# Kernel optimization log

Hardware: AMD Instinct MI355X
Metric: run time of the kernel (lower is better)

The kernel has to match this reference:

```python
import jax, jax.numpy as jnp
import numpy as np

INF = 1.0e9
# 8-connected neighborhood (Warcraft shortest-path convention)
DIRS = [(-1, -1), (-1, 0), (-1, 1), (0, -1), (0, 1), (1, -1), (1, 0), (1, 1)]


def _shifted(d_KGG, di, dj):
    # shifted[i, j] = d[i + di, j + dj], INF out of bounds (di, dj static ints)
    K, G, _ = d_KGG.shape
    p = jnp.pad(d_KGG, ((0, 0), (1, 1), (1, 1)), constant_values=INF)
    return p[:, 1 + di:1 + di + G, 1 + dj:1 + dj + G]


def compute_shortest_path(cost_KGG):
    """Vertex-cost shortest path from (0,0) to (G-1,G-1) on an 8-connected grid.
    Returns a 0/1 mask of cells on the optimal path. Bellman-Ford style DP:
    G*G relaxation sweeps guarantee convergence for positive costs."""
    K, G, _ = cost_KGG.shape
    dist0 = jnp.full((K, G, G), INF, dtype=cost_KGG.dtype).at[:, 0, 0].set(cost_KGG[:, 0, 0])

    def relax(_, dist):
        nbr = dist  # placeholder; fold min over 8 shifted copies
        nbr = _shifted(dist, *DIRS[0])
        for d in DIRS[1:]:
            nbr = jnp.minimum(nbr, _shifted(dist, *d))
        return jnp.minimum(dist, cost_KGG + nbr)

    dist = jax.lax.fori_loop(0, G * G, relax, dist0)

    # Backtrack from (G-1, G-1): predecessor = argmin dist over 8 neighbors.
    di = jnp.array([d[0] for d in DIRS])
    dj = jnp.array([d[1] for d in DIRS])
    ks = jnp.arange(K)

    def step(carry, _):
        mask, pi, pj = carry
        ci = pi[:, None] + di[None, :]   # [K, 8]
        cj = pj[:, None] + dj[None, :]
        valid = (ci >= 0) & (ci < G) & (cj >= 0) & (cj < G)
        cic = jnp.clip(ci, 0, G - 1)
        cjc = jnp.clip(cj, 0, G - 1)
        nd = jnp.where(valid, dist[ks[:, None], cic, cjc], INF)
        best = jnp.argmin(nd, axis=-1)  # [K]
        npi = jnp.take_along_axis(cic, best[:, None], 1)[:, 0]
        npj = jnp.take_along_axis(cjc, best[:, None], 1)[:, 0]
        done = (pi == 0) & (pj == 0)
        pi2 = jnp.where(done, pi, npi)
        pj2 = jnp.where(done, pj, npj)
        mask2 = mask.at[ks, pi2, pj2].set(1.0)
        return (mask2, pi2, pj2), None

    mask0 = jnp.zeros((K, G, G), jnp.float32).at[:, G - 1, G - 1].set(1.0)
    p0 = jnp.full((K,), G - 1, dtype=jnp.int32)
    (mask, _, _), _ = jax.lax.scan(step, (mask0, p0, p0), None, length=G * G)
    return mask


def setup_inputs() -> dict:
    key = jax.random.key(0)
    S, B, G, n_costs = 8, 1024, 12, 5
    w_SBW = jax.random.randint(jax.random.fold_in(key, 1), (S, B, G * G), 0, n_costs)
    costs_t = jnp.array([0.8, 1.2, 5.3, 7.7, 9.2], dtype=jnp.float32)
    return {"w_SBW": w_SBW, "costs_t": costs_t}


def reference(w_SBW, costs_t):
    S, B, W = w_SBW.shape
    G = int(np.sqrt(W))
    w_KGG = w_SBW.reshape(S * B, G, G)
    cost_KGG = costs_t[w_KGG]          # embedding-style gather of per-cell costs
    y_KGG = compute_shortest_path(cost_KGG)
    return y_KGG.reshape(S, B, W).astype(jnp.int32)  # .long() in the original
```

## Files before the change

### kernel.cpp

```cpp
#include <hip/hip_runtime.h>
#include <float.h>

#define GDIM 12
#define NC   144
#define FINF 1.0e9f

__device__ inline float rotA(float x) {
    return __int_as_float(__builtin_amdgcn_update_dpp(
        __float_as_int(x), __float_as_int(x), 0x121, 0xf, 0xf, false));
}
__device__ inline float rotB(float x) {
    return __int_as_float(__builtin_amdgcn_update_dpp(
        __float_as_int(x), __float_as_int(x), 0x12F, 0xf, 0xf, false));
}

#define ROWU(i, TRACK) {                                                   \
    float dm1 = ((i) > 0)        ? d[(i)-1] : FINF;                        \
    float dp1 = ((i) < GDIM - 1) ? d[(i)+1] : FINF;                       \
    float V   = fminf(dm1, dp1);                                           \
    float cm3 = fminf(V, d[(i)]);                                          \
    float nbr = fminf(fminf(rotA(cm3), rotB(cm3)), V);                     \
    float nd  = c[(i)] + nbr;                                              \
    if (TRACK) changed = changed | (nd < d[(i)]);                          \
    d[(i)] = fminf(d[(i)], nd); }

#define RB_SWEEP(TRACK) {                                                  \
    _Pragma("unroll")                                                      \
    for (int i = 0; i < GDIM; i += 2) ROWU(i, TRACK)                       \
    _Pragma("unroll")                                                      \
    for (int i = 1; i < GDIM; i += 2) ROWU(i, TRACK)                       \
}

__device__ __constant__ int POFF[8] = {-15, -14, -13, -1, 1, 13, 14, 15};

__global__ __launch_bounds__(64)
void path_kernel(const int* __restrict__ w,
                 const float* __restrict__ costs,
                 int* __restrict__ out) {
    const int l = threadIdx.x;
    const int g = l >> 4;
    const int j = l & 15;
    const int pbase = blockIdx.x * 4;

    __shared__ int   s_w[4 * NC];
    __shared__ float dl[4][196];
    __shared__ int   ml[4 * NC];

    const int* wblk = w + (size_t)pbase * NC;
    #pragma unroll
    for (int t = 0; t < 9; ++t) { s_w[t * 64 + l] = wblk[t * 64 + l]; ml[t * 64 + l] = 0; }
    {
        float* dlf = &dl[0][0];
        #pragma unroll
        for (int t = 0; t < 13; ++t) { int idx = t * 64 + l; if (idx < 784) dlf[idx] = FINF; }
    }
    __syncthreads();

    const bool act = (j < GDIM);
    float c[GDIM], d[GDIM];
    #pragma unroll
    for (int i = 0; i < GDIM; ++i) {
        c[i] = act ? costs[s_w[g * NC + i * GDIM + j]] : FINF;
        d[i] = FINF;
    }
    if (j == 0) d[0] = c[0];

    for (int pair = 0; pair < 80; ++pair) {
        bool changed = false;
        RB_SWEEP(false)
        RB_SWEEP(true)
        if (__ballot(changed) == 0ull) break;
    }

    if (act) {
        #pragma unroll
        for (int i = 0; i < GDIM; ++i) dl[g][(i + 1) * 14 + (j + 1)] = d[i];
    }
    __syncthreads();

    if (j == 0) {
        int a = 12 * 14 + 12;
        ml[g * NC + NC - 1] = 1;
        int guard = 0;
        while (a != (1 * 14 + 1) && guard < 200) {
            ++guard;
            float best = FLT_MAX; int ba = a;
            #pragma unroll
            for (int dd = 0; dd < 8; ++dd) {
                int na = a + POFF[dd];
                float v = dl[g][na];
                if (v < best) { best = v; ba = na; }
            }
            a = ba;
            int ii = a / 14 - 1, jj = a % 14 - 1;
            ml[g * NC + ii * GDIM + jj] = 1;
        }
    }
    __syncthreads();

    int* outblk = out + (size_t)pbase * NC;
    #pragma unroll
    for (int t = 0; t < 9; ++t) outblk[t * 64 + l] = ml[t * 64 + l];
}

extern "C" void kernel_launch(void* const* d_in, const int* in_sizes, int n_in,
                              void* d_out, int out_size, void* d_ws, size_t ws_size,
                              hipStream_t stream) {
    const int*   w     = (const int*)d_in[0];
    const float* costs = (const float*)d_in[1];
    int*         out   = (int*)d_out;
    const int K = in_sizes[0] / NC;
    path_kernel<<<dim3(K / 4), dim3(64), 0, stream>>>(w, costs, out);
}
```

Measured before the change: 24.43 us.

## Replace red-black relaxation with in-row prefix scans and alternating row sweeps

The relaxation schedule changes from red-black row updates to Gauss-Seidel row sweeps that alternate top-down and bottom-up. Within each row, forward and backward min-plus scans use DPP rotations so distance travels the whole row in one step. Convergence is declared only after two consecutive unchanged sweeps. The aim is fewer outer iterations, paid for with eleven scan steps per row. Global loads and stores are also vectorised to int4.

```diff
diff --git a/kernel.cpp b/kernel.cpp
--- a/kernel.cpp
+++ b/kernel.cpp
@@ -4,6 +4,8 @@
 #define GDIM 12
 #define NC   144
 #define FINF 1.0e9f
+
+__device__ __constant__ int POFF[8] = {-15, -14, -13, -1, 1, 13, 14, 15};
 
 __device__ inline float rotA(float x) {
     return __int_as_float(__builtin_amdgcn_update_dpp(
@@ -14,24 +16,20 @@
         __float_as_int(x), __float_as_int(x), 0x12F, 0xf, 0xf, false));
 }
 
-#define ROWU(i, TRACK) {                                                   \
-    float dm1 = ((i) > 0)        ? d[(i)-1] : FINF;                        \
-    float dp1 = ((i) < GDIM - 1) ? d[(i)+1] : FINF;                       \
-    float V   = fminf(dm1, dp1);                                           \
-    float cm3 = fminf(V, d[(i)]);                                          \
-    float nbr = fminf(fminf(rotA(cm3), rotB(cm3)), V);                     \
-    float nd  = c[(i)] + nbr;                                              \
-    if (TRACK) changed = changed | (nd < d[(i)]);                          \
-    d[(i)] = fminf(d[(i)], nd); }
-
-#define RB_SWEEP(TRACK) {                                                  \
-    _Pragma("unroll")                                                      \
-    for (int i = 0; i < GDIM; i += 2) ROWU(i, TRACK)                       \
-    _Pragma("unroll")                                                      \
-    for (int i = 1; i < GDIM; i += 2) ROWU(i, TRACK)                       \
-}
-
-__device__ __constant__ int POFF[8] = {-15, -14, -13, -1, 1, 13, 14, 15};
+#define ROWFS(i) {                                                        \
+    float uu = fminf(((i) > 0)        ? d[(i) > 0 ? (i)-1 : 0]   : FINF,  \
+                     ((i) < GDIM - 1) ? d[(i) < GDIM-1 ? (i)+1 : GDIM-1] : FINF); \
+    float nbrV = fminf(fminf(rotA(uu), rotB(uu)), uu);                    \
+    float base = fminf(d[(i)], c[(i)] + nbrV);                            \
+    float fF = base, fB = base;                                           \
+    _Pragma("unroll")                                                     \
+    for (int sc = 0; sc < GDIM - 1; ++sc) {                               \
+        fF = fminf(fF, rotA(fF) + c[(i)]);                                \
+        fB = fminf(fB, rotB(fB) + c[(i)]);                                \
+    }                                                                     \
+    float r = fminf(fF, fB);                                              \
+    changed = changed | (r < d[(i)]);                                     \
+    d[(i)] = r; }
 
 __global__ __launch_bounds__(64)
 void path_kernel(const int* __restrict__ w,
@@ -42,13 +40,17 @@
     const int j = l & 15;
     const int pbase = blockIdx.x * 4;
 
-    __shared__ int   s_w[4 * NC];
+    __shared__ int4  s_w4[NC];
     __shared__ float dl[4][196];
-    __shared__ int   ml[4 * NC];
+    __shared__ int4  ml4[NC];
+    int* s_w = (int*)s_w4;
+    int* ml  = (int*)ml4;
 
-    const int* wblk = w + (size_t)pbase * NC;
-    #pragma unroll
-    for (int t = 0; t < 9; ++t) { s_w[t * 64 + l] = wblk[t * 64 + l]; ml[t * 64 + l] = 0; }
+    const int4* wv = (const int4*)(w + (size_t)pbase * NC);
+    const int4 zero4 = make_int4(0, 0, 0, 0);
+    s_w4[l] = wv[l];            ml4[l] = zero4;
+    s_w4[64 + l] = wv[64 + l];  ml4[64 + l] = zero4;
+    if (l < 16) { s_w4[128 + l] = wv[128 + l]; ml4[128 + l] = zero4; }
     {
         float* dlf = &dl[0][0];
         #pragma unroll
@@ -65,11 +67,17 @@
     }
     if (j == 0) d[0] = c[0];
 
-    for (int pair = 0; pair < 80; ++pair) {
+    int clean = 0;
+    for (int s = 0; s < 64 && clean < 2; ++s) {
         bool changed = false;
-        RB_SWEEP(false)
-        RB_SWEEP(true)
-        if (__ballot(changed) == 0ull) break;
+        if ((s & 1) == 0) {
+            #pragma unroll
+            for (int i = 0; i < GDIM; ++i) ROWFS(i)
+        } else {
+            #pragma unroll
+            for (int ii = 0; ii < GDIM; ++ii) { const int i = GDIM - 1 - ii; ROWFS(i) }
+        }
+        clean = (__ballot(changed) == 0ull) ? (clean + 1) : 0;
     }
 
     if (act) {
@@ -98,9 +106,10 @@
     }
     __syncthreads();
 
-    int* outblk = out + (size_t)pbase * NC;
-    #pragma unroll
-    for (int t = 0; t < 9; ++t) outblk[t * 64 + l] = ml[t * 64 + l];
+    int4* ov = (int4*)(out + (size_t)pbase * NC);
+    ov[l] = ml4[l];
+    ov[64 + l] = ml4[64 + l];
+    if (l < 16) ov[128 + l] = ml4[128 + l];
 }
 
 extern "C" void kernel_launch(void* const* d_in, const int* in_sizes, int n_in,
```

Result: slower. 49.39 us (+102.2%).
